# Performance work log

Measured on AMD Instinct MI355X. Metric: run time of the kernel, lower is better.

The kernel has to match this reference:

```python
import jax, jax.numpy as jnp
import numpy as np
from functools import partial

T, B, IN, H = 512, 32, 1024, 1024
NUM_LAYERS = 2
SLOPE, OFFSET = 0.2, 0.5
FORGET_GATE_BIAS = 1.0
W_SCALE = 1.0 / np.sqrt(H)  # mimics reset_parameters uniform(-1/sqrt(H), 1/sqrt(H)) scale


def setup_inputs() -> dict:
    key = jax.random.key(0)
    ks = jax.random.split(key, 12)
    x = jax.random.normal(ks[0], (T, B, IN), dtype=jnp.float32)
    h0 = jax.random.normal(ks[1], (NUM_LAYERS, B, H), dtype=jnp.float32)
    c0 = jax.random.normal(ks[2], (NUM_LAYERS, B, H), dtype=jnp.float32)
    def u(k, shape):
        return jax.random.uniform(k, shape, jnp.float32, -W_SCALE, W_SCALE)
    # layer 0: input_size=IN, layer 1: input_size=H
    W_ih0 = u(ks[3], (4 * H, IN))
    W_hh0 = u(ks[4], (4 * H, H))
    b_ih0 = u(ks[5], (4 * H,)).at[H:2 * H].set(FORGET_GATE_BIAS)
    b_hh0 = u(ks[6], (4 * H,)).at[H:2 * H].set(0.0)
    W_ih1 = u(ks[7], (4 * H, H))
    W_hh1 = u(ks[8], (4 * H, H))
    b_ih1 = u(ks[9], (4 * H,)).at[H:2 * H].set(FORGET_GATE_BIAS)
    b_hh1 = u(ks[10], (4 * H,)).at[H:2 * H].set(0.0)
    return {"x": x, "h0": h0, "c0": c0,
            "W_ih0": W_ih0, "W_hh0": W_hh0, "b_ih0": b_ih0, "b_hh0": b_hh0,
            "W_ih1": W_ih1, "W_hh1": W_hh1, "b_ih1": b_ih1, "b_hh1": b_hh1}


def _hard_sigmoid(g):
    return jnp.clip(SLOPE * g + OFFSET, 0.0, 1.0)


def _hardtanh(g):
    return jnp.clip(g, -1.0, 1.0)


def _run_layer(x, h, c, W_ih, W_hh, b_ih, b_hh):
    """HardLSTMLayerForward: per-step eps = mean(x_t) is added to input and state."""
    def step(carry, xt):
        h, c = carry
        eps = jnp.mean(xt)
        xi = xt + eps          # [B, in]
        hh = h + eps           # [B, H]
        cc = c + eps           # [B, H]
        gates = xi @ W_ih.T + b_ih + hh @ W_hh.T + b_hh  # [B, 4H]
        i_g = _hard_sigmoid(gates[:, :H])
        f_g = _hard_sigmoid(gates[:, H:2 * H])
        g_g = _hardtanh(gates[:, 2 * H:3 * H])
        o_g = _hard_sigmoid(gates[:, 3 * H:])
        cy = f_g * cc + i_g * g_g
        hy = o_g * _hardtanh(cy)
        return (hy, cy), hy
    (h, c), y = jax.lax.scan(step, (h, c), x)
    return y, h, c


def reference(x, h0, c0, W_ih0, W_hh0, b_ih0, b_hh0, W_ih1, W_hh1, b_ih1, b_hh1):
    out = x + 1.0  # StackedLSTM adds `one` to the input
    y0, h_0, c_0 = _run_layer(out, h0[0], c0[0], W_ih0, W_hh0, b_ih0, b_hh0)
    y1, h_1, c_1 = _run_layer(y0, h0[1], c0[1], W_ih1, W_hh1, b_ih1, b_hh1)
    hn = jnp.stack([h_0, h_1])  # [num_layers, B, H]
    cn = jnp.stack([c_0, c_1])
    return (y1, hn, cn)
```

## Files before the change

### kernel.cpp

```cpp
#include <hip/hip_runtime.h>
#include <cstdio>


#define T_STEPS 512
#define DEADLINE_TICKS 6000000ULL

typedef __bf16 bf16x8 __attribute__((ext_vector_type(8)));
typedef float  f32x4  __attribute__((ext_vector_type(4)));
typedef unsigned int u32x4 __attribute__((ext_vector_type(4)));
typedef unsigned long long u64;

#define AGLD(p)   __hip_atomic_load((p), __ATOMIC_RELAXED, __HIP_MEMORY_SCOPE_AGENT)
#define AGST(p,v) __hip_atomic_store((p), (v), __ATOMIC_RELAXED, __HIP_MEMORY_SCOPE_AGENT)
#define MFMA16 __builtin_amdgcn_mfma_f32_16x16x32_bf16

__device__ __forceinline__ u64 rtick(){ return __builtin_amdgcn_s_memrealtime(); }

__device__ __forceinline__ unsigned short f2bf(float f){
  union { float f; unsigned u; } v; v.f = f;
  unsigned r = v.u + 0x7FFFu + ((v.u >> 16) & 1u);
  return (unsigned short)(r >> 16);
}
__device__ __forceinline__ bf16x8 packbf(f32x4 a, f32x4 b){
  unsigned u0 = f2bf(a[0]) | ((unsigned)f2bf(a[1])<<16);
  unsigned u1 = f2bf(a[2]) | ((unsigned)f2bf(a[3])<<16);
  unsigned u2 = f2bf(b[0]) | ((unsigned)f2bf(b[1])<<16);
  unsigned u3 = f2bf(b[2]) | ((unsigned)f2bf(b[3])<<16);
  u32x4 cv = {u0,u1,u2,u3};
  return __builtin_bit_cast(bf16x8, cv);
}
__device__ __forceinline__ int fragOff(int row, int k8){
  return ((k8>>2)*2 + (row>>4))*1024 + ((row&15) | ((k8&3)<<4))*16;
}
__device__ __forceinline__ bf16x8 ld_frag_plain(const char* p){
  u32x4 v = *reinterpret_cast<const u32x4*>(p);
  return __builtin_bit_cast(bf16x8, v);
}
__device__ __forceinline__ bf16x8 lds_frag(const char* p){
  u32x4 v = *reinterpret_cast<const u32x4*>(p);
  return __builtin_bit_cast(bf16x8, v);
}

__device__ __forceinline__ void stage64k_c(const char* src, char* dst, int tid){
  const u32x4* s = reinterpret_cast<const u32x4*>(src) + tid;
  u32x4 r0 = s[0],    r1 = s[256],  r2 = s[512],  r3 = s[768];
  u32x4 r4 = s[1024], r5 = s[1280], r6 = s[1536], r7 = s[1792];
  u32x4 r8 = s[2048], r9 = s[2304], ra = s[2560], rb = s[2816];
  u32x4 rc = s[3072], rd = s[3328], re = s[3584], rf = s[3840];
  u32x4* d = (u32x4*)(dst + tid*16);
  d[0]=r0; d[256]=r1; d[512]=r2; d[768]=r3;
  d[1024]=r4; d[1280]=r5; d[1536]=r6; d[1792]=r7;
  d[2048]=r8; d[2304]=r9; d[2560]=ra; d[2816]=rb;
  d[3072]=rc; d[3328]=rd; d[3584]=re; d[3840]=rf;
}
__device__ __forceinline__ void stage64k_b(const char* src, char* dst, int tid){
  u32x4 r0,r1,r2,r3,r4,r5,r6,r7,r8,r9,ra,rb,rc,rd,re,rf;
  u64 a = (u64)(uintptr_t)src + (u64)tid*16;
  #define LD(reg, off) asm volatile("global_load_dwordx4 %0, %1, off sc0 sc1" \
                                    : "=v"(reg) : "v"(a + (off)) : "memory")
  LD(r0,0); LD(r1,4096); LD(r2,8192); LD(r3,12288);
  LD(r4,16384); LD(r5,20480); LD(r6,24576); LD(r7,28672);
  LD(r8,32768); LD(r9,36864); LD(ra,40960); LD(rb,45056);
  LD(rc,49152); LD(rd,53248); LD(re,57344); LD(rf,61440);
  #undef LD
  asm volatile("s_waitcnt vmcnt(0)" ::: "memory");
  u32x4* d = (u32x4*)(dst + tid*16);
  d[0]=r0; d[256]=r1; d[512]=r2; d[768]=r3;
  d[1024]=r4; d[1280]=r5; d[1536]=r6; d[1792]=r7;
  d[2048]=r8; d[2304]=r9; d[2560]=ra; d[2816]=rb;
  d[3072]=rc; d[3328]=rd; d[3584]=re; d[3840]=rf;
}

__device__ __forceinline__ void spin64(const unsigned short* f, unsigned tgt,
                                       int lane, u64 dl){
  if (lane < 8){
    u64 a = (u64)(uintptr_t)f + (u64)lane*16;
    while (true){
      u32x4 v;
      asm volatile("global_load_dwordx4 %0, %1, off sc0 sc1\n\ts_waitcnt vmcnt(0)"
                   : "=v"(v) : "v"(a) : "memory");
      bool ok = true;
      #pragma unroll
      for (int i=0;i<4;++i){
        unsigned u = v[i];
        ok = ok && ((u & 0xFFFFu) >= tgt) && ((u >> 16) >= tgt);
      }
      if (__all((int)ok)) break;
      if (rtick() > dl) break;
    }
  }
  asm volatile("" ::: "memory");
}


__global__ void prep_xfrag(const float* __restrict__ x, unsigned short* __restrict__ xf){
  int tid = blockIdx.x*256 + threadIdx.x;
  int k8 = tid & 127, row = (tid>>7)&31, t = tid>>12;
  const float* s = x + ((size_t)(t*32+row)*1024 + k8*8);
  f32x4 a = *reinterpret_cast<const f32x4*>(s);
  f32x4 b = *reinterpret_cast<const f32x4*>(s+4);
  f32x4 a1 = {a[0]+1.f,a[1]+1.f,a[2]+1.f,a[3]+1.f};
  f32x4 b1 = {b[0]+1.f,b[1]+1.f,b[2]+1.f,b[3]+1.f};
  bf16x8 v = packbf(a1,b1);
  *reinterpret_cast<bf16x8*>((char*)xf + (size_t)t*65536 + fragOff(row,k8)) = v;
}

__global__ void prep_hfrag(const float* __restrict__ h0, unsigned short* __restrict__ hf){
  int tid = blockIdx.x*256 + threadIdx.x;
  int k8 = tid & 127, row = (tid>>7)&31, L = tid>>12;
  const float* s = h0 + ((size_t)(L*32+row)*1024 + k8*8);
  f32x4 a = *reinterpret_cast<const f32x4*>(s);
  f32x4 b = *reinterpret_cast<const f32x4*>(s+4);
  bf16x8 v = packbf(a,b);
  *reinterpret_cast<bf16x8*>((char*)hf + (size_t)L*65536 + fragOff(row,k8)) = v;
}

__global__ void reduce_mean_f32(const float* __restrict__ src, float* __restrict__ out, float add){
  __shared__ float red[256];
  int t = blockIdx.x, tid = threadIdx.x;
  const float* p = src + (size_t)t*32768;
  float s = 0.f;
  for (int i = tid; i < 32768; i += 256) s += p[i];
  red[tid] = s; __syncthreads();
  for (int o = 128; o > 0; o >>= 1){ if (tid < o) red[tid] += red[tid+o]; __syncthreads(); }
  if (tid == 0) out[t] = red[0]*(1.f/32768.f) + add;
}

__global__ void prep_rs(const float* __restrict__ Wih0, const float* __restrict__ Whh0,
                        const float* __restrict__ Wih1, const float* __restrict__ Whh1,
                        const float* __restrict__ bih0, const float* __restrict__ bhh0,
                        const float* __restrict__ bih1, const float* __restrict__ bhh1,
                        float* __restrict__ rs, float* __restrict__ bias){
  int task = blockIdx.x*4 + (threadIdx.x >> 6);
  int lane = threadIdx.x & 63;
  int L = task >> 12, n = task & 4095;
  const float* pi = (L ? Wih1 : Wih0) + (size_t)n*1024;
  const float* ph = (L ? Whh1 : Whh0) + (size_t)n*1024;
  float s = 0.f;
  #pragma unroll
  for (int e = 0; e < 16; ++e){ int k = lane + e*64; s += pi[k] + ph[k]; }
  #pragma unroll
  for (int m = 32; m; m >>= 1) s += __shfl_xor(s, m);
  if (lane == 0){
    rs[task]   = s;
    bias[task] = (L ? bih1[n] : bih0[n]) + (L ? bhh1[n] : bhh0[n]);
  }
}

__global__ __launch_bounds__(256, 1) void rec12(
    const unsigned short* __restrict__ Xf,
    const unsigned short* __restrict__ HiniF,
    unsigned short* __restrict__ Ring0,
    unsigned short* __restrict__ Ring1,
    int ring1mask, int ring1cached,
    float* __restrict__ out,
    const float* __restrict__ Wih0, const float* __restrict__ Whh0,
    const float* __restrict__ Wih1, const float* __restrict__ Whh1,
    const float* __restrict__ biasC, const float* __restrict__ rsC,
    const float* __restrict__ eps0, const float* __restrict__ c0,
    unsigned* __restrict__ epsP,
    unsigned short* __restrict__ flag0,
    unsigned short* __restrict__ flag1)
{
  __shared__ char ldsA[65536];
  __shared__ char ldsB[65536];

  const int tid  = threadIdx.x;
  const int lane = tid & 63;
  const int w    = tid >> 6;
  const int L    = blockIdx.x >> 6;
  const int bid  = blockIdx.x & 63;
  const int jb   = bid * 16;
  const int jc   = jb + w*4;
  const int c    = lane & 15;
  const int q    = c >> 2;
  const int ncol = q*1024 + jc + (c & 3);
  const int koff = (lane >> 4) << 3;
  const u64 dl   = rtick() + DEADLINE_TICKS;

  __builtin_amdgcn_fence(__ATOMIC_ACQUIRE, "agent");
  __syncthreads();

  const float* Wfirst = L ? Whh1 : Wih0;
  const float* Wsec   = L ? Wih1 : Whh0;

  bf16x8 wregF[32], wregS[32];
  {
    const float* sF = Wfirst + (size_t)ncol*1024 + koff;
    const float* sS = Wsec   + (size_t)ncol*1024 + koff;
    #pragma unroll
    for (int kt = 0; kt < 32; ++kt){
      f32x4 a = *reinterpret_cast<const f32x4*>(sF + kt*32);
      f32x4 b = *reinterpret_cast<const f32x4*>(sF + kt*32 + 4);
      wregF[kt] = packbf(a, b);
      f32x4 cc = *reinterpret_cast<const f32x4*>(sS + kt*32);
      f32x4 d  = *reinterpret_cast<const f32x4*>(sS + kt*32 + 4);
      wregS[kt] = packbf(cc, d);
    }
  }

  const float bia = biasC[L*4096 + ncol];
  const float rsv = rsC[L*4096 + ncol];
  const int jw = jc + (c & 3);
  float creg[2][4];
  #pragma unroll
  for (int m = 0; m < 2; ++m)
    #pragma unroll
    for (int r = 0; r < 4; ++r)
      creg[m][r] = c0[L*32768 + (m*16 + (lane>>4)*4 + r)*1024 + jw];

  float* outHn = out + 16777216 + L*32768;
  float* outCn = out + 16777216 + 65536 + L*32768;
  const u64 myFlagA = (u64)(uintptr_t)((L ? flag1 : flag0) + bid);

  for (int t = 0; t < T_STEPS; ++t){
    f32x4 acc0 = {0.f,0.f,0.f,0.f}, acc1 = {0.f,0.f,0.f,0.f};
    float et;

    if (L == 0){
      const char* Ax = (const char*)Xf + (size_t)t*65536;
      #pragma unroll
      for (int kt = 0; kt < 32; ++kt){
        bf16x8 a0 = ld_frag_plain(Ax + (kt*2 + 0)*1024 + lane*16);
        bf16x8 a1 = ld_frag_plain(Ax + (kt*2 + 1)*1024 + lane*16);
        acc0 = MFMA16(a0, wregF[kt], acc0, 0, 0, 0);
        acc1 = MFMA16(a1, wregF[kt], acc1, 0, 0, 0);
      }
      et = eps0[t];
      if (w == 0 && t > 0) spin64(flag0, (unsigned)t, lane, dl);
      __syncthreads();
      const char* hsrc = (t == 0) ? (const char*)HiniF
                                  : (const char*)Ring0 + (size_t)(t-1)*65536;
      stage64k_c(hsrc, ldsA, tid);
      __syncthreads();
      #pragma unroll
      for (int kt = 0; kt < 32; ++kt){
        bf16x8 a0 = lds_frag(ldsA + (kt*2 + 0)*1024 + lane*16);
        bf16x8 a1 = lds_frag(ldsA + (kt*2 + 1)*1024 + lane*16);
        acc0 = MFMA16(a0, wregS[kt], acc0, 0, 0, 0);
        acc1 = MFMA16(a1, wregS[kt], acc1, 0, 0, 0);
      }
    } else {
      if (w == 0) spin64(flag0, (unsigned)(t+1), lane, dl);
      __syncthreads();
      {
        const u64* ep = reinterpret_cast<const u64*>(epsP + (size_t)t*256) + lane*2;
        u64 v01 = AGLD(ep), v23 = AGLD(ep + 1);
        union { unsigned u; float f; } w0x,w1x,w2x,w3x;
        w0x.u = (unsigned)v01; w1x.u = (unsigned)(v01>>32);
        w2x.u = (unsigned)v23; w3x.u = (unsigned)(v23>>32);
        float bs = ((w0x.f + w1x.f) + w2x.f) + w3x.f;
        int s = (int)llrintf(bs * 65536.f);
        #pragma unroll
        for (int mm = 32; mm; mm >>= 1) s += __shfl_xor(s, mm);
        et = (float)s * 4.6566128730773926e-10f;
      }
      stage64k_c((const char*)Ring0 + (size_t)t*65536, ldsB, tid);
      if (w == 0 && t > 0) spin64(flag1, (unsigned)t, lane, dl);
      __syncthreads();
      const char* hsrc = (t == 0) ? (const char*)HiniF + 65536
                                  : (const char*)Ring1 + (size_t)((t-1) & ring1mask)*65536;
      if (t == 0 || ring1cached) stage64k_c(hsrc, ldsA, tid);
      else                       stage64k_b(hsrc, ldsA, tid);
      __syncthreads();
      #pragma unroll
      for (int kt = 0; kt < 32; ++kt){
        bf16x8 a0 = lds_frag(ldsA + (kt*2 + 0)*1024 + lane*16);
        bf16x8 a1 = lds_frag(ldsA + (kt*2 + 1)*1024 + lane*16);
        acc0 = MFMA16(a0, wregF[kt], acc0, 0, 0, 0);
        acc1 = MFMA16(a1, wregF[kt], acc1, 0, 0, 0);
      }
      #pragma unroll
      for (int kt = 0; kt < 32; ++kt){
        bf16x8 a0 = lds_frag(ldsB + (kt*2 + 0)*1024 + lane*16);
        bf16x8 a1 = lds_frag(ldsB + (kt*2 + 1)*1024 + lane*16);
        acc0 = MFMA16(a0, wregS[kt], acc0, 0, 0, 0);
        acc1 = MFMA16(a1, wregS[kt], acc1, 0, 0, 0);
      }
    }

    char* ringSlot = L ? ((char*)Ring1 + (size_t)(t & ring1mask)*65536)
                       : ((char*)Ring0 + (size_t)t*65536);
    float hyv[2][4];
    float psum = 0.f;
    #pragma unroll
    for (int m = 0; m < 2; ++m){
      f32x4 av = m ? acc1 : acc0;
      #pragma unroll
      for (int r = 0; r < 4; ++r){
        float g  = av[r] + bia + et*rsv;
        float p4 = __shfl_xor(g, 4), p8 = __shfl_xor(g, 8), p12 = __shfl_xor(p4, 8);
        float iv = (q==0)?g:(q==1)?p4:(q==2)?p8:p12;
        float fv = (q==1)?g:(q==0)?p4:(q==3)?p8:p12;
        float gv = (q==2)?g:(q==3)?p4:(q==0)?p8:p12;
        float ov = (q==3)?g:(q==2)?p4:(q==1)?p8:p12;
        iv = fminf(fmaxf(0.2f*iv + 0.5f, 0.f), 1.f);
        fv = fminf(fmaxf(0.2f*fv + 0.5f, 0.f), 1.f);
        gv = fminf(fmaxf(gv, -1.f), 1.f);
        ov = fminf(fmaxf(0.2f*ov + 0.5f, 0.f), 1.f);
        float cc = fv*(creg[m][r] + et) + iv*gv;
        creg[m][r] = cc;
        float hy = ov * fminf(fmaxf(cc, -1.f), 1.f);
        hyv[m][r] = hy;
        if (c < 4) psum += hy;

        unsigned short hu = f2bf(hy);
        unsigned p2 = (unsigned)hu | (((unsigned)__shfl_xor((int)hu, 1)) << 16);
        unsigned q2 = (unsigned)__shfl_xor((int)p2, 2);
        if (c == 0){
          int sub = (lane>>4)*4 + r;
          size_t bo = (size_t)((jc>>5)*2 + m)*1024
                    + (size_t)(sub | (((jc>>3)&3)<<4))*16 + (size_t)(jc&7)*2;
          AGST(reinterpret_cast<u64*>(ringSlot + bo), (u64)p2 | ((u64)q2 << 32));
        }
      }
    }
    if (L == 0){
      #pragma unroll
      for (int mm = 32; mm; mm >>= 1) psum += __shfl_xor(psum, mm);
      if (lane == 0){
        union { float f; unsigned u; } pb; pb.f = psum;
        AGST(epsP + (size_t)t*256 + (bid<<2) + w, pb.u);
      }
    }
    asm volatile("s_waitcnt vmcnt(0)" ::: "memory");
    __syncthreads();
    if (tid == 0)
      asm volatile("global_store_short %0, %1, off sc0 sc1"
                   :: "v"(myFlagA), "v"((unsigned)(t+1)) : "memory");

    if (L){
      #pragma unroll
      for (int m = 0; m < 2; ++m)
        #pragma unroll
        for (int r = 0; r < 4; ++r){
          float hy = hyv[m][r];
          float f1 = __shfl_xor(hy, 1), f2 = __shfl_xor(hy, 2), f3 = __shfl_xor(f1, 2);
          if (c == 0){
            int row = m*16 + (lane>>4)*4 + r;
            f32x4 o4 = {hy, f1, f2, f3};
            *reinterpret_cast<f32x4*>(out + (size_t)t*32768 + row*1024 + jc) = o4;
          }
        }
    }
    if (t == T_STEPS-1){
      #pragma unroll
      for (int m = 0; m < 2; ++m)
        #pragma unroll
        for (int r = 0; r < 4; ++r)
          if (c < 4){
            int row = m*16 + (lane>>4)*4 + r;
            outHn[row*1024 + jw] = hyv[m][r];
            outCn[row*1024 + jw] = creg[m][r];
          }
    }
  }
}


extern "C" void kernel_launch(void* const* d_in, const int* in_sizes, int n_in,
                              void* d_out, int out_size, void* d_ws, size_t ws_size,
                              hipStream_t stream)
{
  const float* x    = (const float*)d_in[0];
  const float* h0   = (const float*)d_in[1];
  const float* c0   = (const float*)d_in[2];
  const float* Wih0 = (const float*)d_in[3];
  const float* Whh0 = (const float*)d_in[4];
  const float* bih0 = (const float*)d_in[5];
  const float* bhh0 = (const float*)d_in[6];
  const float* Wih1 = (const float*)d_in[7];
  const float* Whh1 = (const float*)d_in[8];
  const float* bih1 = (const float*)d_in[9];
  const float* bhh1 = (const float*)d_in[10];
  float* out = (float*)d_out;

  char* ws = (char*)d_ws;
  size_t off = 0;
  auto alloc = [&](size_t bytes)->char* {
    char* p = ws + off; off += (bytes + 255) & ~(size_t)255; return p;
  };
  unsigned short* Xf    = (unsigned short*)alloc((size_t)T_STEPS*65536);
  unsigned short* Ring0 = (unsigned short*)alloc((size_t)T_STEPS*65536);
  unsigned short* HiniF = (unsigned short*)alloc(2*65536);
  float* eps0 = (float*)alloc(T_STEPS*4);
  float* bias = (float*)alloc(2*4096*4);
  float* rs   = (float*)alloc(2*4096*4);
  unsigned* epsP = (unsigned*)alloc((size_t)T_STEPS*256*4);
  char* sync  = alloc(512);
  unsigned short* flag0 = (unsigned short*)sync;
  unsigned short* flag1 = (unsigned short*)(sync + 128);
  size_t remain  = (off <= ws_size) ? (ws_size - off) : 0;
  int r1slots    = (remain >= (size_t)(T_STEPS+1)*65536) ? T_STEPS : 8;
  unsigned short* Ring1 = (unsigned short*)alloc((size_t)r1slots*65536);
  int r1mask   = r1slots - 1;
  int r1cached = (r1slots == T_STEPS) ? 1 : 0;
  if (off > ws_size)
    fprintf(stderr, "HardLSTM: ws too small, need %zu have %zu\n", off, ws_size);

  hipMemsetAsync(sync, 0, 512, stream);
  prep_xfrag<<<8192, 256, 0, stream>>>(x, Xf);
  prep_hfrag<<<32, 256, 0, stream>>>(h0, HiniF);
  reduce_mean_f32<<<T_STEPS, 256, 0, stream>>>(x, eps0, 1.0f);
  prep_rs<<<2048, 256, 0, stream>>>(Wih0, Whh0, Wih1, Whh1,
                                    bih0, bhh0, bih1, bhh1, rs, bias);

  rec12<<<128, 256, 0, stream>>>(Xf, HiniF, Ring0, Ring1, r1mask, r1cached, out,
      Wih0, Whh0, Wih1, Whh1, bias, rs, eps0, c0, epsP, flag0, flag1);
}
```

Before: 6.480 ms.

## Pad sync flags to 128-byte lines and prefetch layer-0 ring into registers

Each block's flag becomes a 32-bit word on its own 128-byte line. Waiters poll with one lane per flag instead of packed 16-bit flags read by 8 lanes, which avoids contention from many writers sharing a cache line. Layer 1 now issues its global loads of the layer-0 output slot into registers before the eps reduction and its own-layer spin wait, then writes them to LDS afterwards, so that load latency overlaps the wait. This costs more registers and a larger flag area.

Measured after the change: 6.275 ms. 1.03x faster.

```diff
diff --git a/kernel.cpp b/kernel.cpp
--- a/kernel.cpp
+++ b/kernel.cpp
@@ -71,23 +71,15 @@
   d[3072]=rc; d[3328]=rd; d[3584]=re; d[3840]=rf;
 }
 
-__device__ __forceinline__ void spin64(const unsigned short* f, unsigned tgt,
-                                       int lane, u64 dl){
-  if (lane < 8){
-    u64 a = (u64)(uintptr_t)f + (u64)lane*16;
-    while (true){
-      u32x4 v;
-      asm volatile("global_load_dwordx4 %0, %1, off sc0 sc1\n\ts_waitcnt vmcnt(0)"
-                   : "=v"(v) : "v"(a) : "memory");
-      bool ok = true;
-      #pragma unroll
-      for (int i=0;i<4;++i){
-        unsigned u = v[i];
-        ok = ok && ((u & 0xFFFFu) >= tgt) && ((u >> 16) >= tgt);
-      }
-      if (__all((int)ok)) break;
-      if (rtick() > dl) break;
-    }
+__device__ __forceinline__ void spin64s(const unsigned* f, unsigned tgt,
+                                        int lane, u64 dl){
+  u64 a = (u64)(uintptr_t)(f + (size_t)lane*32);
+  while (true){
+    unsigned v;
+    asm volatile("global_load_dword %0, %1, off sc0 sc1\n\ts_waitcnt vmcnt(0)"
+                 : "=v"(v) : "v"(a) : "memory");
+    if (__all((int)(v >= tgt))) break;
+    if (rtick() > dl) break;
   }
   asm volatile("" ::: "memory");
 }
@@ -147,7 +139,7 @@
   }
 }
 
-__global__ __launch_bounds__(256, 1) void rec12(
+__global__ __launch_bounds__(256, 1) void rec13(
     const unsigned short* __restrict__ Xf,
     const unsigned short* __restrict__ HiniF,
     unsigned short* __restrict__ Ring0,
@@ -159,8 +151,8 @@
     const float* __restrict__ biasC, const float* __restrict__ rsC,
     const float* __restrict__ eps0, const float* __restrict__ c0,
     unsigned* __restrict__ epsP,
-    unsigned short* __restrict__ flag0,
-    unsigned short* __restrict__ flag1)
+    unsigned* __restrict__ flag0,
+    unsigned* __restrict__ flag1)
 {
   __shared__ char ldsA[65536];
   __shared__ char ldsB[65536];
@@ -211,7 +203,7 @@
 
   float* outHn = out + 16777216 + L*32768;
   float* outCn = out + 16777216 + 65536 + L*32768;
-  const u64 myFlagA = (u64)(uintptr_t)((L ? flag1 : flag0) + bid);
+  const u64 myFlagA = (u64)(uintptr_t)((L ? flag1 : flag0) + (size_t)bid*32);
 
   for (int t = 0; t < T_STEPS; ++t){
     f32x4 acc0 = {0.f,0.f,0.f,0.f}, acc1 = {0.f,0.f,0.f,0.f};
@@ -227,7 +219,7 @@
         acc1 = MFMA16(a1, wregF[kt], acc1, 0, 0, 0);
       }
       et = eps0[t];
-      if (w == 0 && t > 0) spin64(flag0, (unsigned)t, lane, dl);
+      if (w == 0 && t > 0) spin64s(flag0, (unsigned)t, lane, dl);
       __syncthreads();
       const char* hsrc = (t == 0) ? (const char*)HiniF
                                   : (const char*)Ring0 + (size_t)(t-1)*65536;
@@ -241,8 +233,14 @@
         acc1 = MFMA16(a1, wregS[kt], acc1, 0, 0, 0);
       }
     } else {
-      if (w == 0) spin64(flag0, (unsigned)(t+1), lane, dl);
+      if (w == 0) spin64s(flag0, (unsigned)(t+1), lane, dl);
       __syncthreads();
+      const u32x4* sB = reinterpret_cast<const u32x4*>(
+                          (const char*)Ring0 + (size_t)t*65536) + tid;
+      u32x4 b0 = sB[0],    b1 = sB[256],  b2 = sB[512],  b3 = sB[768];
+      u32x4 b4 = sB[1024], b5 = sB[1280], b6 = sB[1536], b7 = sB[1792];
+      u32x4 b8 = sB[2048], b9 = sB[2304], ba = sB[2560], bb = sB[2816];
+      u32x4 bc = sB[3072], bd = sB[3328], be = sB[3584], bf = sB[3840];
       {
         const u64* ep = reinterpret_cast<const u64*>(epsP + (size_t)t*256) + lane*2;
         u64 v01 = AGLD(ep), v23 = AGLD(ep + 1);
@@ -255,9 +253,15 @@
         for (int mm = 32; mm; mm >>= 1) s += __shfl_xor(s, mm);
         et = (float)s * 4.6566128730773926e-10f;
       }
-      stage64k_c((const char*)Ring0 + (size_t)t*65536, ldsB, tid);
-      if (w == 0 && t > 0) spin64(flag1, (unsigned)t, lane, dl);
+      if (w == 0 && t > 0) spin64s(flag1, (unsigned)t, lane, dl);
       __syncthreads();
+      {
+        u32x4* d = (u32x4*)(ldsB + tid*16);
+        d[0]=b0; d[256]=b1; d[512]=b2; d[768]=b3;
+        d[1024]=b4; d[1280]=b5; d[1536]=b6; d[1792]=b7;
+        d[2048]=b8; d[2304]=b9; d[2560]=ba; d[2816]=bb;
+        d[3072]=bc; d[3328]=bd; d[3584]=be; d[3840]=bf;
+      }
       const char* hsrc = (t == 0) ? (const char*)HiniF + 65536
                                   : (const char*)Ring1 + (size_t)((t-1) & ring1mask)*65536;
       if (t == 0 || ring1cached) stage64k_c(hsrc, ldsA, tid);
@@ -326,7 +330,7 @@
     asm volatile("s_waitcnt vmcnt(0)" ::: "memory");
     __syncthreads();
     if (tid == 0)
-      asm volatile("global_store_short %0, %1, off sc0 sc1"
+      asm volatile("global_store_dword %0, %1, off sc0 sc1"
                    :: "v"(myFlagA), "v"((unsigned)(t+1)) : "memory");
 
     if (L){
@@ -387,9 +391,9 @@
   float* bias = (float*)alloc(2*4096*4);
   float* rs   = (float*)alloc(2*4096*4);
   unsigned* epsP = (unsigned*)alloc((size_t)T_STEPS*256*4);
-  char* sync  = alloc(512);
-  unsigned short* flag0 = (unsigned short*)sync;
-  unsigned short* flag1 = (unsigned short*)(sync + 128);
+  char* sync  = alloc(64*128*2);
+  unsigned* flag0 = (unsigned*)sync;
+  unsigned* flag1 = (unsigned*)(sync + 64*128);
   size_t remain  = (off <= ws_size) ? (ws_size - off) : 0;
   int r1slots    = (remain >= (size_t)(T_STEPS+1)*65536) ? T_STEPS : 8;
   unsigned short* Ring1 = (unsigned short*)alloc((size_t)r1slots*65536);
@@ -398,13 +402,13 @@
   if (off > ws_size)
     fprintf(stderr, "HardLSTM: ws too small, need %zu have %zu\n", off, ws_size);
 
-  hipMemsetAsync(sync, 0, 512, stream);
+  hipMemsetAsync(sync, 0, 64*128*2, stream);
   prep_xfrag<<<8192, 256, 0, stream>>>(x, Xf);
   prep_hfrag<<<32, 256, 0, stream>>>(h0, HiniF);
   reduce_mean_f32<<<T_STEPS, 256, 0, stream>>>(x, eps0, 1.0f);
   prep_rs<<<2048, 256, 0, stream>>>(Wih0, Whh0, Wih1, Whh1,
                                     bih0, bhh0, bih1, bhh1, rs, bias);
 
-  rec12<<<128, 256, 0, stream>>>(Xf, HiniF, Ring0, Ring1, r1mask, r1cached, out,
+  rec13<<<128, 256, 0, stream>>>(Xf, HiniF, Ring0, Ring1, r1mask, r1cached, out,
       Wih0, Whh0, Wih1, Whh1, bias, rs, eps0, c0, epsP, flag0, flag1);
 }
```
